# Optimization experiments

Measured on AMD Instinct MI355X. Metric: run time of the kernel, lower is better.

## Reference

```python
import jax, jax.numpy as jnp
import numpy as np

N_ITER = 5
EPS = 1e-20


def setup_inputs() -> dict:
    key = jax.random.key(0)
    k1, k2, k3 = jax.random.split(key, 3)
    M, J, I, K, N = 2, 2048, 2049, 8, 2
    X = jax.random.normal(k1, (M, J, I, 2), dtype=jnp.float32)
    # torch.rand(...) * (1 - 1e-8) + 1e-8  (hoisted out of forward for determinism)
    T0 = jax.random.uniform(k2, (I, K, N), dtype=jnp.float32) * (1 - 1e-8) + 1e-8
    V0 = jax.random.uniform(k3, (K, J, N), dtype=jnp.float32) * (1 - 1e-8) + 1e-8
    return {"X": X, "T0": T0, "V0": V0}


def _ilrma(X_ri, T0, V0):
    # X_ri: (M, J, I, 2) real -> Xc: (I, M, J) complex
    Xp = jnp.transpose(X_ri, (2, 0, 1, 3))
    Xc = jax.lax.complex(Xp[..., 0], Xp[..., 1])
    I_, M, J = Xc.shape
    N = T0.shape[2]
    W = jnp.broadcast_to(jnp.eye(N, M, dtype=Xc.dtype), (I_, N, M))  # (I, N, M)
    Y = jnp.einsum('inm,imj->inj', W, Xc)                            # (I, N, J)
    T, V = T0, V0
    invJ = jnp.asarray(1.0 / J, dtype=Xc.dtype)
    for _ in range(N_ITER):
        for n in range(N):
            Tn = T[:, :, n]            # (I, K)
            Vn = V[:, :, n]            # (K, J)
            Yn = Y[:, n, :]            # (I, J)
            # --- NMF multiplicative updates (vectorized over all I bins) ---
            Rn = Tn @ Vn                                        # (I, J)
            P = jnp.abs(Yn) ** 2 / (jnp.abs(Rn) ** 2 + EPS)     # |Y|^2 / R^2
            Rd = 1.0 / jnp.abs(Rn)                              # 1 / R
            Tn = Tn * jnp.sqrt((P @ Vn.T) / (Rd @ Vn.T))
            Rn = Tn @ Vn
            Vn = Vn * jnp.sqrt((Tn.T @ P) / (Tn.T @ Rd))
            Rn = Tn @ Vn                                        # updated source model
            T = T.at[:, :, n].set(Tn)
            V = V.at[:, :, n].set(Vn)
            # --- demixing vector update, batched over frequency bins I ---
            Xh = Xc / Rn[:, None, :]                            # (I, M, J)
            D = jnp.einsum('imj,ikj->imk', Xh, Xc) * invJ       # (I, M, M) (plain .T, no conj, as in source)
            WD = jnp.einsum('inm,imk->ink', W, D)               # (I, M, M)
            e = jnp.zeros((M,), dtype=Xc.dtype).at[n].set(1.0)
            rhs = jnp.broadcast_to(e[:, None], (I_, M, 1))
            b = jnp.linalg.solve(WD, rhs)[..., 0]               # (I, M)  == inv(W D) @ e_n
            nrm = jnp.einsum('im,imk,ik->i', b, D, b)           # b^T D b (complex, no conj)
            W = W.at[:, :, n].set(b / jnp.sqrt(nrm)[:, None])
        Y = jnp.einsum('inm,imj->inj', W, Xc)
    return Y


def reference(X, T0, V0):
    return _ilrma(X, T0, V0)
```

## Files before the change

kernel.cpp:

```cpp
#include <hip/hip_runtime.h>
#include <math.h>

#define I_  2049
#define J_  2048
#define K_  8
#define N_  2
#define NITER 5
#define EPSF 1e-20f
#define INVJ (1.0/2048.0)
#define CHUNK 16
#define NCHUNK 129

__device__ float4 g_Xc[(size_t)I_*J_];
__device__ float  g_Tt[I_*16];
__device__ float  g_Toldt[I_*16];
__device__ float4 g_Vt4[(size_t)J_*4];
__device__ float2 g_W[I_*4];
__device__ float2 g_Wold[I_*4];
__device__ float4 g_pnA[(size_t)NCHUNK*2*J_];
__device__ float4 g_pnB[(size_t)NCHUNK*2*J_];
__device__ float4 g_pdA[(size_t)NCHUNK*2*J_];
__device__ float4 g_pdB[(size_t)NCHUNK*2*J_];

__device__ __forceinline__ float frcp(float x) { return __builtin_amdgcn_rcpf(x); }

__device__ __forceinline__ float dot44(float4 a, float4 b) {
  return fmaf(a.x, b.x, fmaf(a.y, b.y, fmaf(a.z, b.z, a.w*b.w)));
}
__device__ __forceinline__ float4 f4fma(float s, float4 v, float4 a) {
  a.x = fmaf(s, v.x, a.x); a.y = fmaf(s, v.y, a.y);
  a.z = fmaf(s, v.z, a.z); a.w = fmaf(s, v.w, a.w);
  return a;
}
__device__ __forceinline__ float4 f4add(float4 a, float4 b) {
  return make_float4(a.x+b.x, a.y+b.y, a.z+b.z, a.w+b.w);
}
__device__ __forceinline__ float4 wred4(float4 v) {
  v.x += __shfl_down(v.x,32); v.y += __shfl_down(v.y,32); v.z += __shfl_down(v.z,32); v.w += __shfl_down(v.w,32);
  v.x += __shfl_down(v.x,16); v.y += __shfl_down(v.y,16); v.z += __shfl_down(v.z,16); v.w += __shfl_down(v.w,16);
  v.x += __shfl_down(v.x, 8); v.y += __shfl_down(v.y, 8); v.z += __shfl_down(v.z, 8); v.w += __shfl_down(v.w, 8);
  v.x += __shfl_down(v.x, 4); v.y += __shfl_down(v.y, 4); v.z += __shfl_down(v.z, 4); v.w += __shfl_down(v.w, 4);
  v.x += __shfl_down(v.x, 2); v.y += __shfl_down(v.y, 2); v.z += __shfl_down(v.z, 2); v.w += __shfl_down(v.w, 2);
  v.x += __shfl_down(v.x, 1); v.y += __shfl_down(v.y, 1); v.z += __shfl_down(v.z, 1); v.w += __shfl_down(v.w, 1);
  return v;
}
#define RW(x) { x += __shfl_down(x,32); x += __shfl_down(x,16); x += __shfl_down(x,8); \
                x += __shfl_down(x,4);  x += __shfl_down(x,2);  x += __shfl_down(x,1); }

struct dcx { double x, y; };
__device__ __forceinline__ dcx cmul(dcx a, dcx b) { return {a.x*b.x - a.y*b.y, a.x*b.y + a.y*b.x}; }
__device__ __forceinline__ dcx cadd(dcx a, dcx b) { return {a.x + b.x, a.y + b.y}; }
__device__ __forceinline__ dcx csub(dcx a, dcx b) { return {a.x - b.x, a.y - b.y}; }
__device__ __forceinline__ dcx cneg(dcx a) { return {-a.x, -a.y}; }
__device__ __forceinline__ dcx cdiv(dcx a, dcx b) {
  double d = b.x*b.x + b.y*b.y;
  return {(a.x*b.x + a.y*b.y)/d, (a.y*b.x - a.x*b.y)/d};
}
__device__ __forceinline__ dcx csqrt_(dcx z) {
  double r = hypot(z.x, z.y);
  if (r == 0.0) return {0.0, 0.0};
  double t = sqrt(0.5*(r + fabs(z.x)));
  if (z.x >= 0.0) return {t, z.y/(2.0*t)};
  return {fabs(z.y)/(2.0*t), (z.y >= 0.0) ? t : -t};
}

__device__ __forceinline__ float2 cyn(float2 w0, float2 w1, float2 x0, float2 x1) {
  float2 y;
  y.x = w0.x*x0.x - w0.y*x0.y + w1.x*x1.x - w1.y*x1.y;
  y.y = w0.x*x0.y + w0.y*x0.x + w1.x*x1.y + w1.y*x1.x;
  return y;
}

__device__ __forceinline__ void solve12(int i, const double* s_, float2* wout) {
  dcx Wl[2][2];
  Wl[0][0] = {g_W[(size_t)i*4+0].x, g_W[(size_t)i*4+0].y};
  Wl[0][1] = {g_W[(size_t)i*4+1].x, g_W[(size_t)i*4+1].y};
  Wl[1][0] = {g_W[(size_t)i*4+2].x, g_W[(size_t)i*4+2].y};
  Wl[1][1] = {g_W[(size_t)i*4+3].x, g_W[(size_t)i*4+3].y};
#pragma unroll
  for (int n = 0; n < N_; n++) {
    dcx D00 = {s_[6*n+0]*INVJ, s_[6*n+1]*INVJ};
    dcx D01 = {s_[6*n+2]*INVJ, s_[6*n+3]*INVJ};
    dcx D11 = {s_[6*n+4]*INVJ, s_[6*n+5]*INVJ};
    dcx WD00 = cadd(cmul(Wl[0][0], D00), cmul(Wl[0][1], D01));
    dcx WD01 = cadd(cmul(Wl[0][0], D01), cmul(Wl[0][1], D11));
    dcx WD10 = cadd(cmul(Wl[1][0], D00), cmul(Wl[1][1], D01));
    dcx WD11 = cadd(cmul(Wl[1][0], D01), cmul(Wl[1][1], D11));
    dcx det = csub(cmul(WD00, WD11), cmul(WD01, WD10));
    dcx b0, b1;
    if (n == 0) { b0 = cdiv(WD11, det);        b1 = cdiv(cneg(WD10), det); }
    else        { b0 = cdiv(cneg(WD01), det);  b1 = cdiv(WD00, det); }
    dcx nrm = cadd(cmul(cmul(b0, b0), D00), cmul(cmul(b1, b1), D11));
    dcx tcr = cmul(cmul(b0, b1), D01); tcr.x *= 2.0; tcr.y *= 2.0;
    nrm = cadd(nrm, tcr);
    dcx sq = csqrt_(nrm);
    Wl[0][n] = cdiv(b0, sq);
    Wl[1][n] = cdiv(b1, sq);
  }
  float2 o00 = make_float2((float)Wl[0][0].x, (float)Wl[0][0].y);
  float2 o01 = make_float2((float)Wl[0][1].x, (float)Wl[0][1].y);
  float2 o10 = make_float2((float)Wl[1][0].x, (float)Wl[1][0].y);
  float2 o11 = make_float2((float)Wl[1][1].x, (float)Wl[1][1].y);
  g_W[(size_t)i*4+0] = o00; g_W[(size_t)i*4+1] = o01;
  g_W[(size_t)i*4+2] = o10; g_W[(size_t)i*4+3] = o11;
  g_Wold[(size_t)i*4+0] = o00; g_Wold[(size_t)i*4+1] = o01;
  g_Wold[(size_t)i*4+2] = o10; g_Wold[(size_t)i*4+3] = o11;
  wout[0] = o00; wout[1] = o01; wout[2] = o10; wout[3] = o11;
}

__global__ __launch_bounds__(256) void k_setup(const float* __restrict__ T0,
                                               const float* __restrict__ V0) {
  int idx = blockIdx.x*256 + threadIdx.x;
  if (idx < I_*K_) {
    int i = idx >> 3, k = idx & 7;
    float2 v = ((const float2*)T0)[idx];
    g_Tt[i*16 + k]     = v.x;
    g_Tt[i*16 + 8 + k] = v.y;
  }
  if (idx < K_*J_) {
    int k = idx >> 11, j = idx & (J_-1);
    float2 v = ((const float2*)V0)[idx];
    float* vtf = (float*)g_Vt4;
    vtf[j*16 + k]     = v.x;
    vtf[j*16 + 8 + k] = v.y;
  }
  if (idx < I_*4) {
    int r = (idx >> 1) & 1, c = idx & 1;
    float2 v = make_float2((r == c) ? 1.f : 0.f, 0.f);
    g_W[idx] = v;
    g_Wold[idx] = v;
  }
}

__global__ __launch_bounds__(256) void k_transpose(const float* __restrict__ X) {
  __shared__ float2 s0[32][65];
  __shared__ float2 s1[32][65];
  int i0 = blockIdx.x*64, j0 = blockIdx.y*32;
  int lane = threadIdx.x & 63, row = threadIdx.x >> 6;
  const float2* X2 = (const float2*)X;
  int gi = i0 + lane;
  if (gi < I_) {
    for (int jj = row; jj < 32; jj += 4) {
      s0[jj][lane] = X2[(size_t)(0*J_ + j0 + jj)*I_ + gi];
      s1[jj][lane] = X2[(size_t)(1*J_ + j0 + jj)*I_ + gi];
    }
  }
  __syncthreads();
  int jj = threadIdx.x & 31, ii0 = threadIdx.x >> 5;
  for (int u = 0; u < 8; u++) {
    int ii = ii0*8 + u;
    int i = i0 + ii;
    if (i < I_) {
      float2 a = s0[jj][ii], b = s1[jj][ii];
      g_Xc[(size_t)i*J_ + j0 + jj] = make_float4(a.x, a.y, b.x, b.y);
    }
  }
}

__global__ __launch_bounds__(256, 2) void k_tv(int doD) {
  int i = blockIdx.x, t = threadIdx.x;
  int wv = t >> 6, lane = t & 63;
  __shared__ float redD[4][12];
  __shared__ float2 sW[4];
  __shared__ float redT[4][32];

  const float4* T4 = (const float4*)g_Tt;
  float4 tt0 = T4[i*4+0], tt1 = T4[i*4+1];
  float4 tt2 = T4[i*4+2], tt3 = T4[i*4+3];

  size_t xb = (size_t)i*J_ + wv*512 + lane;
  float4 xv0 = g_Xc[xb+0*64], xv1 = g_Xc[xb+1*64], xv2 = g_Xc[xb+2*64], xv3 = g_Xc[xb+3*64];
  float4 xv4 = g_Xc[xb+4*64], xv5 = g_Xc[xb+5*64], xv6 = g_Xc[xb+6*64], xv7 = g_Xc[xb+7*64];

  if (doD) {
    float s0=0.f,s1=0.f,s2=0.f,s3=0.f,s4=0.f,s5=0.f,s6=0.f,s7=0.f,s8=0.f,s9=0.f,s10=0.f,s11=0.f;
#define DB(U) { int j = wv*512 + U*64 + lane; \
    const float4* Vp = g_Vt4 + (size_t)j*4; \
    float4 vt0=Vp[0], vt1=Vp[1], vt2=Vp[2], vt3=Vp[3]; \
    float rn0 = dot44(tt0,vt0)+dot44(tt1,vt1); \
    float rn1 = dot44(tt2,vt2)+dot44(tt3,vt3); \
    float a0=xv##U.x, b0=xv##U.y, a1=xv##U.z, b1=xv##U.w; \
    float e00r=a0*a0-b0*b0, e00i=2.f*a0*b0; \
    float e01r=a0*a1-b0*b1, e01i=a0*b1+a1*b0; \
    float e11r=a1*a1-b1*b1, e11i=2.f*a1*b1; \
    float inv0=frcp(rn0), inv1=frcp(rn1); \
    s0=fmaf(e00r,inv0,s0);  s1=fmaf(e00i,inv0,s1); \
    s2=fmaf(e01r,inv0,s2);  s3=fmaf(e01i,inv0,s3); \
    s4=fmaf(e11r,inv0,s4);  s5=fmaf(e11i,inv0,s5); \
    s6=fmaf(e00r,inv1,s6);  s7=fmaf(e00i,inv1,s7); \
    s8=fmaf(e01r,inv1,s8);  s9=fmaf(e01i,inv1,s9); \
    s10=fmaf(e11r,inv1,s10); s11=fmaf(e11i,inv1,s11); }
    DB(0) DB(1) DB(2) DB(3) DB(4) DB(5) DB(6) DB(7)
#undef DB
    RW(s0) RW(s1) RW(s2) RW(s3) RW(s4) RW(s5) RW(s6) RW(s7) RW(s8) RW(s9) RW(s10) RW(s11)
    if (lane == 0) {
      redD[wv][0]=s0;  redD[wv][1]=s1;  redD[wv][2]=s2;  redD[wv][3]=s3;
      redD[wv][4]=s4;  redD[wv][5]=s5;  redD[wv][6]=s6;  redD[wv][7]=s7;
      redD[wv][8]=s8;  redD[wv][9]=s9;  redD[wv][10]=s10; redD[wv][11]=s11;
    }
    __syncthreads();
    if (t == 0) {
      double s_[12];
#pragma unroll
      for (int q = 0; q < 12; q++)
        s_[q] = (double)redD[0][q] + (double)redD[1][q] + (double)redD[2][q] + (double)redD[3][q];
      float2 w[4];
      solve12(i, s_, w);
      sW[0] = w[0]; sW[1] = w[1]; sW[2] = w[2]; sW[3] = w[3];
    }
  } else {
    if (t == 0) {
      sW[0] = g_Wold[(size_t)i*4+0]; sW[1] = g_Wold[(size_t)i*4+1];
      sW[2] = g_Wold[(size_t)i*4+2]; sW[3] = g_Wold[(size_t)i*4+3];
    }
  }
  __syncthreads();
  float2 w00 = sW[0], w01 = sW[1], w10 = sW[2], w11 = sW[3];

  float4 z = make_float4(0.f,0.f,0.f,0.f);
  float4 aN0a=z, aN0b=z, aD0a=z, aD0b=z, aN1a=z, aN1b=z, aD1a=z, aD1b=z;
#define TB(U) { int j = wv*512 + U*64 + lane; \
  const float4* Vp = g_Vt4 + (size_t)j*4; \
  float4 vt0=Vp[0], vt1=Vp[1], vt2=Vp[2], vt3=Vp[3]; \
  float rn0 = dot44(tt0,vt0)+dot44(tt1,vt1); \
  float rn1 = dot44(tt2,vt2)+dot44(tt3,vt3); \
  float2 x0=make_float2(xv##U.x,xv##U.y), x1=make_float2(xv##U.z,xv##U.w); \
  float2 y0=cyn(w00,w01,x0,x1), y1=cyn(w10,w11,x0,x1); \
  float p0=(y0.x*y0.x+y0.y*y0.y)*frcp(rn0*rn0+EPSF); \
  float p1=(y1.x*y1.x+y1.y*y1.y)*frcp(rn1*rn1+EPSF); \
  float rd0=frcp(rn0), rd1=frcp(rn1); \
  aN0a=f4fma(p0,vt0,aN0a); aN0b=f4fma(p0,vt1,aN0b); \
  aD0a=f4fma(rd0,vt0,aD0a); aD0b=f4fma(rd0,vt1,aD0b); \
  aN1a=f4fma(p1,vt2,aN1a); aN1b=f4fma(p1,vt3,aN1b); \
  aD1a=f4fma(rd1,vt2,aD1a); aD1b=f4fma(rd1,vt3,aD1b); }
  TB(0) TB(1) TB(2) TB(3) TB(4) TB(5) TB(6) TB(7)
#undef TB
  aN0a = wred4(aN0a); aN0b = wred4(aN0b); aD0a = wred4(aD0a); aD0b = wred4(aD0b);
  aN1a = wred4(aN1a); aN1b = wred4(aN1b); aD1a = wred4(aD1a); aD1b = wred4(aD1b);
  if (lane == 0) {
    redT[wv][0]=aN0a.x;  redT[wv][1]=aN0a.y;  redT[wv][2]=aN0a.z;  redT[wv][3]=aN0a.w;
    redT[wv][4]=aN0b.x;  redT[wv][5]=aN0b.y;  redT[wv][6]=aN0b.z;  redT[wv][7]=aN0b.w;
    redT[wv][8]=aD0a.x;  redT[wv][9]=aD0a.y;  redT[wv][10]=aD0a.z; redT[wv][11]=aD0a.w;
    redT[wv][12]=aD0b.x; redT[wv][13]=aD0b.y; redT[wv][14]=aD0b.z; redT[wv][15]=aD0b.w;
    redT[wv][16]=aN1a.x; redT[wv][17]=aN1a.y; redT[wv][18]=aN1a.z; redT[wv][19]=aN1a.w;
    redT[wv][20]=aN1b.x; redT[wv][21]=aN1b.y; redT[wv][22]=aN1b.z; redT[wv][23]=aN1b.w;
    redT[wv][24]=aD1a.x; redT[wv][25]=aD1a.y; redT[wv][26]=aD1a.z; redT[wv][27]=aD1a.w;
    redT[wv][28]=aD1b.x; redT[wv][29]=aD1b.y; redT[wv][30]=aD1b.z; redT[wv][31]=aD1b.w;
  }
  __syncthreads();
  if (t < 8) {
    int k = t;
    float n0 = redT[0][k]    + redT[1][k]    + redT[2][k]    + redT[3][k];
    float d0 = redT[0][8+k]  + redT[1][8+k]  + redT[2][8+k]  + redT[3][8+k];
    float n1 = redT[0][16+k] + redT[1][16+k] + redT[2][16+k] + redT[3][16+k];
    float d1 = redT[0][24+k] + redT[1][24+k] + redT[2][24+k] + redT[3][24+k];
    float tvx = g_Tt[i*16 + k], tvy = g_Tt[i*16 + 8 + k];
    g_Toldt[i*16 + k]     = tvx;
    g_Toldt[i*16 + 8 + k] = tvy;
    g_Tt[i*16 + k]     = tvx * sqrtf(n0/d0);
    g_Tt[i*16 + 8 + k] = tvy * sqrtf(n1/d1);
  }
}

__global__ __launch_bounds__(256, 2) void k_vupd2() {
  int t  = threadIdx.x;
  int j  = blockIdx.x*256 + t;
  int c  = blockIdx.y;
  int i0 = c*CHUNK;
  int ni = I_ - i0; if (ni > CHUNK) ni = CHUNK;

  __shared__ float2 sWold[CHUNK*4];
  __shared__ float4 sTold[CHUNK*4];
  __shared__ float4 sT[CHUNK*4];
  const float4* To4 = (const float4*)g_Toldt;
  const float4* Tn4 = (const float4*)g_Tt;
  if (t < CHUNK*4) {
    int g = i0*4 + t; if (g < I_*4) sWold[t] = g_Wold[g];
  } else if (t < CHUNK*8) {
    int u = t - CHUNK*4; int g = i0*4 + u; if (g < I_*4) sTold[u] = To4[g];
  } else if (t < CHUNK*12) {
    int u = t - CHUNK*8; int g = i0*4 + u; if (g < I_*4) sT[u] = Tn4[g];
  }
  __syncthreads();

  const float4* Vp = g_Vt4 + (size_t)j*4;
  float4 vt0 = Vp[0], vt1 = Vp[1], vt2 = Vp[2], vt3 = Vp[3];
  float4 z = make_float4(0.f,0.f,0.f,0.f);
  float4 aN0a=z, aN0b=z, aD0a=z, aD0b=z, aN1a=z, aN1b=z, aD1a=z, aD1b=z;

  auto body = [&](int ii, float4 xv) {
    float2 x0 = make_float2(xv.x, xv.y), x1 = make_float2(xv.z, xv.w);
    float2 w00 = sWold[ii*4+0], w01 = sWold[ii*4+1], w10 = sWold[ii*4+2], w11 = sWold[ii*4+3];
    float4 to0 = sTold[ii*4+0], to1 = sTold[ii*4+1], to2 = sTold[ii*4+2], to3 = sTold[ii*4+3];
    float rn0 = dot44(to0,vt0)+dot44(to1,vt1);
    float rn1 = dot44(to2,vt2)+dot44(to3,vt3);
    float2 y0 = cyn(w00,w01,x0,x1), y1 = cyn(w10,w11,x0,x1);
    float p0 = (y0.x*y0.x+y0.y*y0.y)*frcp(rn0*rn0+EPSF);
    float p1 = (y1.x*y1.x+y1.y*y1.y)*frcp(rn1*rn1+EPSF);
    float rd0 = frcp(rn0), rd1 = frcp(rn1);
    float4 st0 = sT[ii*4+0], st1 = sT[ii*4+1], st2 = sT[ii*4+2], st3 = sT[ii*4+3];
    aN0a = f4fma(p0,  st0, aN0a); aN0b = f4fma(p0,  st1, aN0b);
    aD0a = f4fma(rd0, st0, aD0a); aD0b = f4fma(rd0, st1, aD0b);
    aN1a = f4fma(p1,  st2, aN1a); aN1b = f4fma(p1,  st3, aN1b);
    aD1a = f4fma(rd1, st2, aD1a); aD1b = f4fma(rd1, st3, aD1b);
  };

  int ii = 0;
  for (; ii + 8 <= ni; ii += 8) {
    float4 xA = g_Xc[(size_t)(i0+ii+0)*J_ + j];
    float4 xB = g_Xc[(size_t)(i0+ii+1)*J_ + j];
    float4 xC = g_Xc[(size_t)(i0+ii+2)*J_ + j];
    float4 xD = g_Xc[(size_t)(i0+ii+3)*J_ + j];
    float4 xE = g_Xc[(size_t)(i0+ii+4)*J_ + j];
    float4 xF = g_Xc[(size_t)(i0+ii+5)*J_ + j];
    float4 xG = g_Xc[(size_t)(i0+ii+6)*J_ + j];
    float4 xH = g_Xc[(size_t)(i0+ii+7)*J_ + j];
    body(ii+0,xA); body(ii+1,xB); body(ii+2,xC); body(ii+3,xD);
    body(ii+4,xE); body(ii+5,xF); body(ii+6,xG); body(ii+7,xH);
  }
  for (; ii < ni; ii++) body(ii, g_Xc[(size_t)(i0+ii)*J_ + j]);

  size_t b2 = (size_t)c*2*J_;
  g_pnA[b2 + j] = aN0a;  g_pnA[b2 + J_ + j] = aN0b;
  g_pnB[b2 + j] = aN1a;  g_pnB[b2 + J_ + j] = aN1b;
  g_pdA[b2 + j] = aD0a;  g_pdA[b2 + J_ + j] = aD0b;
  g_pdB[b2 + j] = aD1a;  g_pdB[b2 + J_ + j] = aD1b;
}

__global__ __launch_bounds__(256) void k_vapply2() {
  int t = threadIdx.x;
  int g = blockIdx.x*16 + (t & 15);
  int slice = t >> 4;
  int kg = g >> 11, j = g & (J_-1);
  int c0 = slice*9, c1 = c0 + 9; if (c1 > NCHUNK) c1 = NCHUNK;
  float4 z = make_float4(0.f,0.f,0.f,0.f);
  float4 sNa=z, sNb=z, sDa=z, sDb=z;
  for (int c = c0; c < c1; c++) {
    size_t o = (size_t)c*2*J_ + (size_t)kg*J_ + j;
    sNa = f4add(sNa, g_pnA[o]); sNb = f4add(sNb, g_pnB[o]);
    sDa = f4add(sDa, g_pdA[o]); sDb = f4add(sDb, g_pdB[o]);
  }
  __shared__ float4 rNa[16][16], rNb[16][16], rDa[16][16], rDb[16][16];
  rNa[slice][t & 15] = sNa; rNb[slice][t & 15] = sNb;
  rDa[slice][t & 15] = sDa; rDb[slice][t & 15] = sDb;
  __syncthreads();
  if (t < 16) {
    float4 na = rNa[0][t], nb = rNb[0][t], da = rDa[0][t], db = rDb[0][t];
#pragma unroll
    for (int s = 1; s < 16; s++) {
      na = f4add(na, rNa[s][t]); nb = f4add(nb, rNb[s][t]);
      da = f4add(da, rDa[s][t]); db = f4add(db, rDb[s][t]);
    }
    int gg = blockIdx.x*16 + t;
    int kg2 = gg >> 11, j2 = gg & (J_-1);
    float4 v0 = g_Vt4[(size_t)j2*4 + kg2];
    float4 v1 = g_Vt4[(size_t)j2*4 + 2 + kg2];
    v0.x *= sqrtf(na.x/da.x); v0.y *= sqrtf(na.y/da.y); v0.z *= sqrtf(na.z/da.z); v0.w *= sqrtf(na.w/da.w);
    v1.x *= sqrtf(nb.x/db.x); v1.y *= sqrtf(nb.y/db.y); v1.z *= sqrtf(nb.z/db.z); v1.w *= sqrtf(nb.w/db.w);
    g_Vt4[(size_t)j2*4 + kg2] = v0;
    g_Vt4[(size_t)j2*4 + 2 + kg2] = v1;
  }
}

__global__ __launch_bounds__(256, 2) void k_yout(float* __restrict__ out, int cplx) {
  int i = blockIdx.x, t = threadIdx.x;
  int wv = t >> 6, lane = t & 63;
  __shared__ float redD[4][12];
  __shared__ float2 sW[4];

  const float4* T4 = (const float4*)g_Tt;
  float4 tt0 = T4[i*4+0], tt1 = T4[i*4+1], tt2 = T4[i*4+2], tt3 = T4[i*4+3];

  size_t xb = (size_t)i*J_ + wv*512 + lane;
  float4 xv0 = g_Xc[xb+0*64], xv1 = g_Xc[xb+1*64], xv2 = g_Xc[xb+2*64], xv3 = g_Xc[xb+3*64];
  float4 xv4 = g_Xc[xb+4*64], xv5 = g_Xc[xb+5*64], xv6 = g_Xc[xb+6*64], xv7 = g_Xc[xb+7*64];

  {
    float s0=0.f,s1=0.f,s2=0.f,s3=0.f,s4=0.f,s5=0.f,s6=0.f,s7=0.f,s8=0.f,s9=0.f,s10=0.f,s11=0.f;
#define DB(U) { int j = wv*512 + U*64 + lane; \
    const float4* Vp = g_Vt4 + (size_t)j*4; \
    float4 vt0=Vp[0], vt1=Vp[1], vt2=Vp[2], vt3=Vp[3]; \
    float rn0 = dot44(tt0,vt0)+dot44(tt1,vt1); \
    float rn1 = dot44(tt2,vt2)+dot44(tt3,vt3); \
    float a0=xv##U.x, b0=xv##U.y, a1=xv##U.z, b1=xv##U.w; \
    float e00r=a0*a0-b0*b0, e00i=2.f*a0*b0; \
    float e01r=a0*a1-b0*b1, e01i=a0*b1+a1*b0; \
    float e11r=a1*a1-b1*b1, e11i=2.f*a1*b1; \
    float inv0=frcp(rn0), inv1=frcp(rn1); \
    s0=fmaf(e00r,inv0,s0);  s1=fmaf(e00i,inv0,s1); \
    s2=fmaf(e01r,inv0,s2);  s3=fmaf(e01i,inv0,s3); \
    s4=fmaf(e11r,inv0,s4);  s5=fmaf(e11i,inv0,s5); \
    s6=fmaf(e00r,inv1,s6);  s7=fmaf(e00i,inv1,s7); \
    s8=fmaf(e01r,inv1,s8);  s9=fmaf(e01i,inv1,s9); \
    s10=fmaf(e11r,inv1,s10); s11=fmaf(e11i,inv1,s11); }
    DB(0) DB(1) DB(2) DB(3) DB(4) DB(5) DB(6) DB(7)
#undef DB
    RW(s0) RW(s1) RW(s2) RW(s3) RW(s4) RW(s5) RW(s6) RW(s7) RW(s8) RW(s9) RW(s10) RW(s11)
    if (lane == 0) {
      redD[wv][0]=s0;  redD[wv][1]=s1;  redD[wv][2]=s2;  redD[wv][3]=s3;
      redD[wv][4]=s4;  redD[wv][5]=s5;  redD[wv][6]=s6;  redD[wv][7]=s7;
      redD[wv][8]=s8;  redD[wv][9]=s9;  redD[wv][10]=s10; redD[wv][11]=s11;
    }
  }
  __syncthreads();
  if (t == 0) {
    double s_[12];
#pragma unroll
    for (int q = 0; q < 12; q++)
      s_[q] = (double)redD[0][q] + (double)redD[1][q] + (double)redD[2][q] + (double)redD[3][q];
    float2 w[4];
    solve12(i, s_, w);
    sW[0] = w[0]; sW[1] = w[1]; sW[2] = w[2]; sW[3] = w[3];
  }
  __syncthreads();
  float2 w00 = sW[0], w01 = sW[1], w10 = sW[2], w11 = sW[3];
  float2* out2 = (float2*)out;
#define YB(U) { int j = wv*512 + U*64 + lane; \
  float2 x0 = make_float2(xv##U.x, xv##U.y); \
  float2 x1 = make_float2(xv##U.z, xv##U.w); \
  float2 y0 = cyn(w00, w01, x0, x1); \
  float2 y1 = cyn(w10, w11, x0, x1); \
  if (cplx) { \
    out2[((size_t)i*N_ + 0)*J_ + j] = y0; \
    out2[((size_t)i*N_ + 1)*J_ + j] = y1; \
  } else { \
    out[((size_t)i*N_ + 0)*J_ + j] = y0.x; \
    out[((size_t)i*N_ + 1)*J_ + j] = y1.x; \
  } }
  YB(0) YB(1) YB(2) YB(3) YB(4) YB(5) YB(6) YB(7)
#undef YB
}

extern "C" void kernel_launch(void* const* d_in, const int* in_sizes, int n_in,
                              void* d_out, int out_size, void* d_ws, size_t ws_size,
                              hipStream_t stream) {
  const float* X  = (const float*)d_in[0];
  const float* T0 = (const float*)d_in[1];
  const float* V0 = (const float*)d_in[2];
  (void)d_ws; (void)ws_size;

  k_setup<<<(I_*K_ + 255)/256, 256, 0, stream>>>(T0, V0);
  k_transpose<<<dim3((I_ + 63)/64, J_/32), 256, 0, stream>>>(X);

  int cplx = (out_size >= 2*I_*N_*J_) ? 1 : 0;
  for (int it = 0; it < NITER; it++) {
    k_tv<<<I_, 256, 0, stream>>>(it > 0);
    k_vupd2<<<dim3(J_/256, NCHUNK), 256, 0, stream>>>();
    k_vapply2<<<2*J_/16, 256, 0, stream>>>();
  }
  k_yout<<<I_, 256, 0, stream>>>((float*)d_out, cplx);
}
```

Before: 536.0 us.

## Stage X tiles in shared memory and double the V-update chunk size

In k_tv and k_yout, the eight float4 X values per thread are written to LDS and re-read after the solve barrier, so they do not have to stay live in registers across the D reduction. This is meant to cut register pressure and spills. The k_vupd2 chunk grows from 16 to 32 frequency bins, which halves the partial-sum buffers and the reduction work in k_vapply2, with the loader loop and slice bounds adjusted to match. In exchange, each block uses 32KB of LDS, which may limit occupancy, and each V-update block has fewer parallel blocks to spread across.

```diff
diff --git a/kernel.cpp b/kernel.cpp
--- a/kernel.cpp
+++ b/kernel.cpp
@@ -8,8 +8,8 @@
 #define NITER 5
 #define EPSF 1e-20f
 #define INVJ (1.0/2048.0)
-#define CHUNK 16
-#define NCHUNK 129
+#define CHUNK 32
+#define NCHUNK 65
 
 __device__ float4 g_Xc[(size_t)I_*J_];
 __device__ float  g_Tt[I_*16];
@@ -160,6 +160,7 @@
 __global__ __launch_bounds__(256, 2) void k_tv(int doD) {
   int i = blockIdx.x, t = threadIdx.x;
   int wv = t >> 6, lane = t & 63;
+  __shared__ float4 sXc[8][256];
   __shared__ float redD[4][12];
   __shared__ float2 sW[4];
   __shared__ float redT[4][32];
@@ -171,6 +172,8 @@
   size_t xb = (size_t)i*J_ + wv*512 + lane;
   float4 xv0 = g_Xc[xb+0*64], xv1 = g_Xc[xb+1*64], xv2 = g_Xc[xb+2*64], xv3 = g_Xc[xb+3*64];
   float4 xv4 = g_Xc[xb+4*64], xv5 = g_Xc[xb+5*64], xv6 = g_Xc[xb+6*64], xv7 = g_Xc[xb+7*64];
+  sXc[0][t] = xv0; sXc[1][t] = xv1; sXc[2][t] = xv2; sXc[3][t] = xv3;
+  sXc[4][t] = xv4; sXc[5][t] = xv5; sXc[6][t] = xv6; sXc[7][t] = xv7;
 
   if (doD) {
     float s0=0.f,s1=0.f,s2=0.f,s3=0.f,s4=0.f,s5=0.f,s6=0.f,s7=0.f,s8=0.f,s9=0.f,s10=0.f,s11=0.f;
@@ -222,9 +225,10 @@
 #define TB(U) { int j = wv*512 + U*64 + lane; \
   const float4* Vp = g_Vt4 + (size_t)j*4; \
   float4 vt0=Vp[0], vt1=Vp[1], vt2=Vp[2], vt3=Vp[3]; \
+  float4 xl = sXc[U][t]; \
   float rn0 = dot44(tt0,vt0)+dot44(tt1,vt1); \
   float rn1 = dot44(tt2,vt2)+dot44(tt3,vt3); \
-  float2 x0=make_float2(xv##U.x,xv##U.y), x1=make_float2(xv##U.z,xv##U.w); \
+  float2 x0=make_float2(xl.x,xl.y), x1=make_float2(xl.z,xl.w); \
   float2 y0=cyn(w00,w01,x0,x1), y1=cyn(w10,w11,x0,x1); \
   float p0=(y0.x*y0.x+y0.y*y0.y)*frcp(rn0*rn0+EPSF); \
   float p1=(y1.x*y1.x+y1.y*y1.y)*frcp(rn1*rn1+EPSF); \
@@ -274,12 +278,14 @@
   __shared__ float4 sT[CHUNK*4];
   const float4* To4 = (const float4*)g_Toldt;
   const float4* Tn4 = (const float4*)g_Tt;
-  if (t < CHUNK*4) {
-    int g = i0*4 + t; if (g < I_*4) sWold[t] = g_Wold[g];
-  } else if (t < CHUNK*8) {
-    int u = t - CHUNK*4; int g = i0*4 + u; if (g < I_*4) sTold[u] = To4[g];
-  } else if (t < CHUNK*12) {
-    int u = t - CHUNK*8; int g = i0*4 + u; if (g < I_*4) sT[u] = Tn4[g];
+  for (int u = t; u < CHUNK*12; u += 256) {
+    if (u < CHUNK*4) {
+      int g = i0*4 + u;               if (g < I_*4) sWold[u] = g_Wold[g];
+    } else if (u < CHUNK*8) {
+      int v = u - CHUNK*4; int g = i0*4 + v; if (g < I_*4) sTold[v] = To4[g];
+    } else {
+      int v = u - CHUNK*8; int g = i0*4 + v; if (g < I_*4) sT[v] = Tn4[g];
+    }
   }
   __syncthreads();
 
@@ -332,7 +338,7 @@
   int g = blockIdx.x*16 + (t & 15);
   int slice = t >> 4;
   int kg = g >> 11, j = g & (J_-1);
-  int c0 = slice*9, c1 = c0 + 9; if (c1 > NCHUNK) c1 = NCHUNK;
+  int c0 = slice*5, c1 = c0 + 5; if (c1 > NCHUNK) c1 = NCHUNK; if (c0 > NCHUNK) c0 = NCHUNK;
   float4 z = make_float4(0.f,0.f,0.f,0.f);
   float4 sNa=z, sNb=z, sDa=z, sDb=z;
   for (int c = c0; c < c1; c++) {
@@ -365,6 +371,7 @@
 __global__ __launch_bounds__(256, 2) void k_yout(float* __restrict__ out, int cplx) {
   int i = blockIdx.x, t = threadIdx.x;
   int wv = t >> 6, lane = t & 63;
+  __shared__ float4 sXc[8][256];
   __shared__ float redD[4][12];
   __shared__ float2 sW[4];
 
@@ -374,6 +381,8 @@
   size_t xb = (size_t)i*J_ + wv*512 + lane;
   float4 xv0 = g_Xc[xb+0*64], xv1 = g_Xc[xb+1*64], xv2 = g_Xc[xb+2*64], xv3 = g_Xc[xb+3*64];
   float4 xv4 = g_Xc[xb+4*64], xv5 = g_Xc[xb+5*64], xv6 = g_Xc[xb+6*64], xv7 = g_Xc[xb+7*64];
+  sXc[0][t] = xv0; sXc[1][t] = xv1; sXc[2][t] = xv2; sXc[3][t] = xv3;
+  sXc[4][t] = xv4; sXc[5][t] = xv5; sXc[6][t] = xv6; sXc[7][t] = xv7;
 
   {
     float s0=0.f,s1=0.f,s2=0.f,s3=0.f,s4=0.f,s5=0.f,s6=0.f,s7=0.f,s8=0.f,s9=0.f,s10=0.f,s11=0.f;
@@ -416,8 +425,9 @@
   float2 w00 = sW[0], w01 = sW[1], w10 = sW[2], w11 = sW[3];
   float2* out2 = (float2*)out;
 #define YB(U) { int j = wv*512 + U*64 + lane; \
-  float2 x0 = make_float2(xv##U.x, xv##U.y); \
-  float2 x1 = make_float2(xv##U.z, xv##U.w); \
+  float4 xl = sXc[U][t]; \
+  float2 x0 = make_float2(xl.x, xl.y); \
+  float2 x1 = make_float2(xl.z, xl.w); \
   float2 y0 = cyn(w00, w01, x0, x1); \
   float2 y1 = cyn(w10, w11, x0, x1); \
   if (cplx) { \
```

Result: faster. 514.2 us (-4.1%).
